# Optimization experiments

Hardware: AMD Instinct MI355X
Metric: run time of the kernel (lower is better)

## Reference

```python
import jax, jax.numpy as jnp
import numpy as np

NUM_USERS = 200000
NUM_ITEMS = 100000
N = NUM_USERS + NUM_ITEMS
EMB_DIM = 64
NUM_LAYERS = 3
NNZ = 4000000


def setup_inputs() -> dict:
    key = jax.random.key(0)
    k1, k2, k3, k4, k5 = jax.random.split(key, 5)
    # xavier_uniform: bound = sqrt(6/(fan_in+fan_out))
    bound = float(np.sqrt(6.0 / (NUM_USERS + EMB_DIM)))
    user_emb = jax.random.uniform(k1, (NUM_USERS, EMB_DIM), jnp.float32, -bound, bound)
    bound_i = float(np.sqrt(6.0 / (NUM_ITEMS + EMB_DIM)))
    item_emb = jax.random.uniform(k2, (NUM_ITEMS, EMB_DIM), jnp.float32, -bound_i, bound_i)
    rows = jax.random.randint(k3, (NNZ,), 0, N, dtype=jnp.int32)
    cols = jax.random.randint(k4, (NNZ,), 0, N, dtype=jnp.int32)
    vals = jax.random.uniform(k5, (NNZ,), jnp.float32)
    return {"user_emb": user_emb, "item_emb": item_emb,
            "rows": rows, "cols": cols, "vals": vals}


def _spmm(rows, cols, vals, x):
    # sparse (N,N) @ dense (N,D) via gather + segment-sum scatter
    gathered = vals[:, None] * x[cols]          # [nnz, D]
    return jax.ops.segment_sum(gathered, rows, num_segments=N)


def reference(user_emb, item_emb, rows, cols, vals):
    emb = jnp.concatenate([user_emb, item_emb], axis=0)  # [N, D]
    acc = emb  # running sum fuses the layer-mean (avoids stacking all layers)
    for _ in range(NUM_LAYERS):
        emb = _spmm(rows, cols, vals, emb)
        acc = acc + emb
    final = acc / (NUM_LAYERS + 1)
    return final[:NUM_USERS], final[NUM_USERS:]
```

## Files before the change

### kernel.cpp

```cpp
#include <hip/hip_runtime.h>


#define NUSERS 200000
#define NITEMS 100000
#define NNODES 300000
#define DIM 64
#define NNZ_CNT 4000000

#define BSHIFT 10
#define BROWS  (1 << BSHIFT)
#define NB     ((NNODES + BROWS - 1) >> BSHIFT)
#define EPB    8192


__device__ __forceinline__ unsigned short f32_to_bf16(float f) {
    unsigned u = __float_as_uint(f);
    u += 0x7FFFu + ((u >> 16) & 1u);
    return (unsigned short)(u >> 16);
}
__device__ __forceinline__ float bf16_to_f32(unsigned short h) {
    return __uint_as_float(((unsigned)h) << 16);
}


__global__ void __launch_bounds__(256) k_bhist(const int* __restrict__ rows,
                                               int* __restrict__ bcnt) {
    __shared__ int hist[NB];
    int t = threadIdx.x;
    int e0 = blockIdx.x * EPB;
    for (int i = t; i < NB; i += 256) hist[i] = 0;
    __syncthreads();
    for (int k = 0; k < EPB / 256; ++k) {
        int e = e0 + k * 256 + t;
        if (e < NNZ_CNT) atomicAdd(&hist[rows[e] >> BSHIFT], 1);
    }
    __syncthreads();
    for (int i = t; i < NB; i += 256) {
        int h = hist[i];
        if (h) atomicAdd(&bcnt[i], h);
    }
}

__global__ void k_bscan(const int* __restrict__ bcnt, int* __restrict__ bbase,
                        int* __restrict__ gcur) {
    int t = threadIdx.x;
    int v = (t < NB) ? bcnt[t] : 0;
    __shared__ int lds[512];
    lds[t] = v; __syncthreads();
    for (int d = 1; d < 512; d <<= 1) {
        int cur = lds[t];
        int add = (t >= d) ? lds[t - d] : 0;
        __syncthreads();
        lds[t] = cur + add;
        __syncthreads();
    }
    if (t < NB) {
        int e = lds[t] - v;
        bbase[t] = e;
        gcur[t]  = e;
    }
    if (t == 511) bbase[NB] = lds[511];
}


__global__ void __launch_bounds__(256) k_bucketA(
        const int* __restrict__ rows, const int* __restrict__ cols,
        const float* __restrict__ vals, int* __restrict__ gcursor,
        int2* __restrict__ staged) {
    __shared__ int hist[NB];
    __shared__ int lbase[NB];
    __shared__ int lcur[NB];
    int t = threadIdx.x;
    int e0 = blockIdx.x * EPB;
    for (int i = t; i < NB; i += 256) { hist[i] = 0; lcur[i] = 0; }
    __syncthreads();
    for (int k = 0; k < EPB / 256; ++k) {
        int e = e0 + k * 256 + t;
        if (e < NNZ_CNT) atomicAdd(&hist[rows[e] >> BSHIFT], 1);
    }
    __syncthreads();
    for (int i = t; i < NB; i += 256) {
        int h = hist[i];
        lbase[i] = h ? atomicAdd(&gcursor[i], h) : 0;
    }
    __syncthreads();
    for (int k = 0; k < EPB / 256; ++k) {
        int e = e0 + k * 256 + t;
        if (e >= NNZ_CNT) continue;
        int r = rows[e];
        int b = r >> BSHIFT;
        int p = lbase[b] + atomicAdd(&lcur[b], 1);
        int2 rec;
        rec.x = ((r & (BROWS - 1)) << 19) | cols[e];
        rec.y = __float_as_int(vals[e]);
        staged[p] = rec;
    }
}


__global__ void __launch_bounds__(1024) k_bucketB(
        const int* __restrict__ bbase, const int2* __restrict__ staged,
        int2* __restrict__ packed, int* __restrict__ rowptr) {
    __shared__ int rcnt[BROWS];
    __shared__ int cur[BROWS];
    int b = blockIdx.x;
    int t = threadIdx.x;
    int r0 = b << BSHIFT;
    int r1 = min(r0 + BROWS, NNODES);
    int nrows = r1 - r0;
    rcnt[t] = 0;
    __syncthreads();
    int start = bbase[b];
    int end   = bbase[b + 1];
    const int* sx = (const int*)staged;
    for (int idx = start + t; idx < end; idx += 1024)
        atomicAdd(&rcnt[((unsigned)sx[idx << 1]) >> 19], 1);
    __syncthreads();
    int v = rcnt[t];
    for (int d = 1; d < 1024; d <<= 1) {
        int c = rcnt[t];
        int a = (t >= d) ? rcnt[t - d] : 0;
        __syncthreads();
        rcnt[t] = c + a;
        __syncthreads();
    }
    int excl = rcnt[t] - v;
    cur[t] = start + excl;
    if (t < nrows) rowptr[r0 + t] = start + excl;
    if (b == NB - 1 && t == 0) rowptr[NNODES] = end;
    __syncthreads();
    for (int idx = start + t; idx < end; idx += 1024) {
        int2 rec = staged[idx];
        int rel = ((unsigned)rec.x) >> 19;
        int col = rec.x & 0x7FFFF;
        int pos = atomicAdd(&cur[rel], 1);
        int2 out; out.x = col; out.y = rec.y;
        packed[pos] = out;
    }
}


__global__ void k_init0(const float* __restrict__ ue, const float* __restrict__ ie,
                        unsigned short* __restrict__ xb0) {
    int i = blockIdx.x * blockDim.x + threadIdx.x;
    const int total = NNODES * DIM / 4;
    if (i >= total) return;
    const int userEnd = NUSERS * DIM / 4;
    float4 v = (i < userEnd) ? ((const float4*)ue)[i]
                             : ((const float4*)ie)[i - userEnd];
    ushort4 h;
    h.x = f32_to_bf16(v.x); h.y = f32_to_bf16(v.y);
    h.z = f32_to_bf16(v.z); h.w = f32_to_bf16(v.w);
    ((ushort4*)xb0)[i] = h;
}


template <int FINAL>
__global__ void __launch_bounds__(256) k_spmm(
        const int* __restrict__ rowptr, const int2* __restrict__ packed,
        const unsigned short* __restrict__ xin,
        unsigned short* __restrict__ y,
        const unsigned short* __restrict__ xprev,
        const float* __restrict__ ue, const float* __restrict__ ie,
        float* __restrict__ out) {
    int row  = blockIdx.x * (blockDim.x >> 6) + (threadIdx.x >> 6);
    int lane = threadIdx.x & 63;
    if (row >= NNODES) return;
    int start = __builtin_amdgcn_readfirstlane(rowptr[row]);
    int end   = __builtin_amdgcn_readfirstlane(rowptr[row + 1]);
    const unsigned short* __restrict__ xl = xin + lane;
    float s0 = 0.f, s1 = 0.f, s2 = 0.f, s3 = 0.f;
    for (int base = start; base < end; base += 16) {
        int2 e[16];
        #pragma unroll
        for (int j = 0; j < 16; ++j) e[j] = packed[base + j];
        float g[16];
        #pragma unroll
        for (int j = 0; j < 16; ++j)
            g[j] = bf16_to_f32(xl[(size_t)e[j].x << 6]);
        #pragma unroll
        for (int j = 0; j < 16; ++j) {
            float v = (base + j < end) ? __int_as_float(e[j].y) : 0.0f;
            float p = v * g[j];
            if ((j & 3) == 0) s0 += p;
            else if ((j & 3) == 1) s1 += p;
            else if ((j & 3) == 2) s2 += p;
            else s3 += p;
        }
    }
    float s = (s0 + s1) + (s2 + s3);
    size_t o = ((size_t)row << 6) + lane;
    if (FINAL) {
        float x0 = (row < NUSERS) ? ue[o] : ie[o - (size_t)NUSERS * DIM];
        float x1 = bf16_to_f32(xprev[o]);
        float x2 = bf16_to_f32(xin[o]);
        out[o] = (x0 + x1 + x2 + s) * 0.25f;
    } else {
        y[o] = f32_to_bf16(s);
    }
}


extern "C" void kernel_launch(void* const* d_in, const int* in_sizes, int n_in,
                              void* d_out, int out_size, void* d_ws, size_t ws_size,
                              hipStream_t stream) {
    const float* ue   = (const float*)d_in[0];
    const float* ie   = (const float*)d_in[1];
    const int*   rows = (const int*)d_in[2];
    const int*   cols = (const int*)d_in[3];
    const float* vals = (const float*)d_in[4];
    float* out = (float*)d_out;

    const size_t embN = (size_t)NNODES * DIM;
    char* p = (char*)d_ws;
    unsigned short* xb0 = (unsigned short*)p;  p += embN * 2;
    unsigned short* xb1 = (unsigned short*)p;  p += embN * 2;
    unsigned short* xb2 = (unsigned short*)p;  p += embN * 2;
    int*   rowptr = (int*)p;              p += (size_t)(NNODES + 16) * 4;
    int*   bcnt   = (int*)p;              p += 512 * 4;
    int*   bbase  = (int*)p;              p += 512 * 4;
    int*   gcur   = (int*)p;              p += 512 * 4;
    int2*  staged = (int2*)p;             p += (size_t)NNZ_CNT * 8;
    int2*  packed = (int2*)p;             p += (size_t)(NNZ_CNT + 16) * 8;

    const int row_blocks  = (NNODES + 3) / 4;
    const int edge_hblocks = (NNZ_CNT + EPB - 1) / EPB;
    const int vec_blocks = (NNODES * DIM / 4 + 255) / 256;

    hipMemsetAsync(bcnt, 0, 512 * 4, stream);
    hipMemsetAsync(packed + NNZ_CNT, 0, 16 * sizeof(int2), stream);
    k_bhist<<<edge_hblocks, 256, 0, stream>>>(rows, bcnt);
    k_bscan<<<1, 512, 0, stream>>>(bcnt, bbase, gcur);

    k_bucketA<<<edge_hblocks, 256, 0, stream>>>(rows, cols, vals, gcur, staged);
    k_bucketB<<<NB, 1024, 0, stream>>>(bbase, staged, packed, rowptr);

    k_init0<<<vec_blocks, 256, 0, stream>>>(ue, ie, xb0);

    k_spmm<0><<<row_blocks, 256, 0, stream>>>(rowptr, packed, xb0, xb1,
                                              (const unsigned short*)nullptr, ue, ie, (float*)nullptr);
    k_spmm<0><<<row_blocks, 256, 0, stream>>>(rowptr, packed, xb1, xb2,
                                              (const unsigned short*)nullptr, ue, ie, (float*)nullptr);
    k_spmm<1><<<row_blocks, 256, 0, stream>>>(rowptr, packed, xb2, (unsigned short*)nullptr,
                                              xb1, ue, ie, out);
}
```

Measured before the change: 735.8 us.

## Gather four bf16 features per lane, processing four edges per wave step

The SpMM gather is restructured so each wavefront splits into four 16-lane groups. Each group handles a different edge and loads 8 bytes (four bf16 features) per lane, so one instruction covers four neighbor rows instead of one. Partial sums across the groups are combined with cross-lane shuffles, and 16 lanes then write vectorized outputs. This cuts the number of gather instructions and makes memory requests wider, at the cost of shuffle reductions and lane-select logic.

Result: slower. 2.193 ms (+198.0%).

```diff
diff --git a/kernel.cpp b/kernel.cpp
--- a/kernel.cpp
+++ b/kernel.cpp
@@ -20,6 +20,12 @@
 }
 __device__ __forceinline__ float bf16_to_f32(unsigned short h) {
     return __uint_as_float(((unsigned)h) << 16);
+}
+__device__ __forceinline__ float bf16_lo(unsigned u) {
+    return __uint_as_float(u << 16);
+}
+__device__ __forceinline__ float bf16_hi(unsigned u) {
+    return __uint_as_float(u & 0xFFFF0000u);
 }
 
 
@@ -166,37 +172,56 @@
     int row  = blockIdx.x * (blockDim.x >> 6) + (threadIdx.x >> 6);
     int lane = threadIdx.x & 63;
     if (row >= NNODES) return;
+    int grp = lane >> 4;
+    int sub = lane & 15;
     int start = __builtin_amdgcn_readfirstlane(rowptr[row]);
     int end   = __builtin_amdgcn_readfirstlane(rowptr[row + 1]);
-    const unsigned short* __restrict__ xl = xin + lane;
-    float s0 = 0.f, s1 = 0.f, s2 = 0.f, s3 = 0.f;
+    const uint2* __restrict__ xq = (const uint2*)xin;
+    float a0 = 0.f, a1 = 0.f, a2 = 0.f, a3 = 0.f;
     for (int base = start; base < end; base += 16) {
         int2 e[16];
         #pragma unroll
         for (int j = 0; j < 16; ++j) e[j] = packed[base + j];
-        float g[16];
         #pragma unroll
-        for (int j = 0; j < 16; ++j)
-            g[j] = bf16_to_f32(xl[(size_t)e[j].x << 6]);
-        #pragma unroll
-        for (int j = 0; j < 16; ++j) {
-            float v = (base + j < end) ? __int_as_float(e[j].y) : 0.0f;
-            float p = v * g[j];
-            if ((j & 3) == 0) s0 += p;
-            else if ((j & 3) == 1) s1 += p;
-            else if ((j & 3) == 2) s2 += p;
-            else s3 += p;
+        for (int q = 0; q < 4; ++q) {
+            int k = q * 4;
+            int c01 = (grp & 1) ? e[k + 1].x : e[k + 0].x;
+            int c23 = (grp & 1) ? e[k + 3].x : e[k + 2].x;
+            int c   = (grp & 2) ? c23 : c01;
+            float v01 = (grp & 1) ? __int_as_float(e[k + 1].y) : __int_as_float(e[k + 0].y);
+            float v23 = (grp & 1) ? __int_as_float(e[k + 3].y) : __int_as_float(e[k + 2].y);
+            float v   = (grp & 2) ? v23 : v01;
+            v = (base + k + grp < end) ? v : 0.0f;
+            uint2 d = xq[((size_t)c << 4) + sub];
+            a0 += v * bf16_lo(d.x);
+            a1 += v * bf16_hi(d.x);
+            a2 += v * bf16_lo(d.y);
+            a3 += v * bf16_hi(d.y);
         }
     }
-    float s = (s0 + s1) + (s2 + s3);
-    size_t o = ((size_t)row << 6) + lane;
-    if (FINAL) {
-        float x0 = (row < NUSERS) ? ue[o] : ie[o - (size_t)NUSERS * DIM];
-        float x1 = bf16_to_f32(xprev[o]);
-        float x2 = bf16_to_f32(xin[o]);
-        out[o] = (x0 + x1 + x2 + s) * 0.25f;
-    } else {
-        y[o] = f32_to_bf16(s);
+    a0 += __shfl_xor(a0, 16); a0 += __shfl_xor(a0, 32);
+    a1 += __shfl_xor(a1, 16); a1 += __shfl_xor(a1, 32);
+    a2 += __shfl_xor(a2, 16); a2 += __shfl_xor(a2, 32);
+    a3 += __shfl_xor(a3, 16); a3 += __shfl_xor(a3, 32);
+    if (lane < 16) {
+        size_t ro = (size_t)row * 16 + sub;
+        if (FINAL) {
+            float4 x0 = (row < NUSERS) ? ((const float4*)ue)[ro]
+                                       : ((const float4*)ie)[ro - (size_t)NUSERS * 16];
+            ushort4 h1 = ((const ushort4*)xprev)[ro];
+            ushort4 h2 = ((const ushort4*)xin)[ro];
+            float4 r;
+            r.x = (x0.x + bf16_to_f32(h1.x) + bf16_to_f32(h2.x) + a0) * 0.25f;
+            r.y = (x0.y + bf16_to_f32(h1.y) + bf16_to_f32(h2.y) + a1) * 0.25f;
+            r.z = (x0.z + bf16_to_f32(h1.z) + bf16_to_f32(h2.z) + a2) * 0.25f;
+            r.w = (x0.w + bf16_to_f32(h1.w) + bf16_to_f32(h2.w) + a3) * 0.25f;
+            ((float4*)out)[ro] = r;
+        } else {
+            ushort4 h;
+            h.x = f32_to_bf16(a0); h.y = f32_to_bf16(a1);
+            h.z = f32_to_bf16(a2); h.w = f32_to_bf16(a3);
+            ((ushort4*)y)[ro] = h;
+        }
     }
 }
 
```
